# Kernel optimization log

Hardware: AMD Instinct MI355X
Metric: run time of the kernel (lower is better)

## Reference

```python
import jax, jax.numpy as jnp
import numpy as np

N, D, C, P = 4096, 512, 100, 64
EPS_COS = 1e-8   # torch cosine_similarity norm clamp
EPS_INV = 1e-5   # module's 1/(d + 1e-5)


def setup_inputs() -> dict:
    key = jax.random.key(0)
    k1, k2, k3, k4 = jax.random.split(key, 4)
    feats = jax.random.normal(k1, (N, D), dtype=jnp.float32)
    protos = jax.random.normal(k2, (C, P, D), dtype=jnp.float32)
    cls_ids = jax.random.randint(k3, (N,), 0, C)
    proto_labels = jax.random.randint(k4, (C, P), 0, 1000)
    return {"feats": feats, "protos": protos, "cls_ids": cls_ids,
            "proto_labels": proto_labels}


def reference(feats, protos, cls_ids, proto_labels):
    # Gather each box's class-conditional prototype set: [N, P, D]
    p = protos[cls_ids]
    pl = proto_labels[cls_ids]                       # [N, P]

    # cosine distance: 1 - f.p / (max(|f|,eps) * max(|p|,eps))
    dot = jnp.einsum('nd,npd->np', feats, p)         # [N, P]
    fnorm = jnp.maximum(jnp.linalg.norm(feats, axis=-1, keepdims=True), EPS_COS)
    pnorm = jnp.maximum(jnp.linalg.norm(p, axis=-1), EPS_COS)
    d_cos = 1.0 - dot / (fnorm * pnorm)

    diff = feats[:, None, :] - p                     # [N, P, D]
    d_l1 = jnp.mean(jnp.abs(diff), axis=-1)          # F.l1_loss (mean)
    d_l2 = jnp.mean(diff * diff, axis=-1)            # F.mse_loss (mean)

    dists = jnp.stack([d_cos, d_l1, d_l2], axis=1)   # [N, 3, P]
    probs = jax.nn.softmax(1.0 / (dists + EPS_INV), axis=-1).mean(axis=1)  # [N, P]

    idx = jnp.argmax(probs, axis=-1)                 # [N]
    labels = jnp.take_along_axis(pl, idx[:, None], axis=1)[:, 0]
    return labels, probs
```

## Files before the change

kernel.cpp:

```cpp
#include <hip/hip_runtime.h>

#define D 512
#define P 64
#define CHUNK 16
#define MAXDESC 512
#define EPS_COS 1e-8f
#define EPS_INV 1e-5f


__device__ __forceinline__ float wave_sum(float v) {
#pragma unroll
    for (int m = 32; m >= 1; m >>= 1) v += __shfl_xor(v, m, 64);
    return v;
}

__global__ __launch_bounds__(256) void proto_norm_kernel(
    const float* __restrict__ protos, float* __restrict__ pp, int rows)
{
    const int lane = threadIdx.x & 63;
    const int r = blockIdx.x * 4 + (threadIdx.x >> 6);
    if (r >= rows) return;
    const float* row = protos + (size_t)r * D;
    const float4 a = *(const float4*)(row + lane * 4);
    const float4 b = *(const float4*)(row + 256 + lane * 4);
    float s = a.x*a.x + a.y*a.y + a.z*a.z + a.w*a.w
            + b.x*b.x + b.y*b.y + b.z*b.z + b.w*b.w;
    s = wave_sum(s);
    if (lane == 0) pp[r] = s;
}

__global__ __launch_bounds__(256) void hist_kernel(
    const int* __restrict__ cls, int* counts, int N)
{
    const int n = blockIdx.x * 256 + threadIdx.x;
    if (n < N) atomicAdd(&counts[cls[n]], 1);
}

__global__ __launch_bounds__(64) void scan_desc_kernel(
    const int* __restrict__ counts, int* base, int* desc, int* ndesc, int C)
{
    const int lane = threadIdx.x;
    const int c0 = lane, c1 = lane + 64;
    const int v0 = (c0 < C) ? counts[c0] : 0;
    const int v1 = (c1 < C) ? counts[c1] : 0;
    int s0 = v0, s1 = v1;
#pragma unroll
    for (int d = 1; d < 64; d <<= 1) {
        int t = __shfl_up(s0, d, 64); if (lane >= d) s0 += t;
        t     = __shfl_up(s1, d, 64); if (lane >= d) s1 += t;
    }
    s1 += __shfl(s0, 63, 64);
    const int b0 = s0 - v0, b1 = s1 - v1;
    if (c0 < C) base[c0] = b0;
    if (c1 < C) base[c1] = b1;

    const int g0 = (v0 + CHUNK - 1) / CHUNK, g1 = (v1 + CHUNK - 1) / CHUNK;
    int t0 = g0, t1 = g1;
#pragma unroll
    for (int d = 1; d < 64; d <<= 1) {
        int t = __shfl_up(t0, d, 64); if (lane >= d) t0 += t;
        t     = __shfl_up(t1, d, 64); if (lane >= d) t1 += t;
    }
    t1 += __shfl(t0, 63, 64);
    const int go0 = t0 - g0, go1 = t1 - g1;
    if (lane == 63) ndesc[0] = t1;
    for (int k = 0; k < g0; ++k) {
        const int di = go0 + k;
        desc[3*di] = c0; desc[3*di+1] = b0 + CHUNK*k; desc[3*di+2] = min(CHUNK, v0 - CHUNK*k);
    }
    for (int k = 0; k < g1; ++k) {
        const int di = go1 + k;
        desc[3*di] = c1; desc[3*di+1] = b1 + CHUNK*k; desc[3*di+2] = min(CHUNK, v1 - CHUNK*k);
    }
}

__global__ __launch_bounds__(256) void scatter_kernel(
    const int* __restrict__ cls, const int* __restrict__ base,
    int* fill, int* sorted, int N)
{
    const int n = blockIdx.x * 256 + threadIdx.x;
    if (n < N) {
        const int c = cls[n];
        const int pos = base[c] + atomicAdd(&fill[c], 1);
        sorted[pos] = n;
    }
}

__global__ __launch_bounds__(256, 2) void proto_main_kernel(
    const float* __restrict__ feats,
    const float* __restrict__ protos,
    const int*   __restrict__ proto_labels,
    const float* __restrict__ ppbuf,
    const int*   __restrict__ sorted,
    const int*   __restrict__ desc,
    const int*   __restrict__ ndesc,
    float* __restrict__ out, int N)
{
    __shared__ float tile[32 * D];
    const int nd = ndesc[0];
    if ((int)blockIdx.x >= nd) return;
    const int cls   = desc[3*blockIdx.x];
    const int start = desc[3*blockIdx.x+1];
    const int cnt   = desc[3*blockIdx.x+2];
    const int lane = threadIdx.x & 63;
    const int wave = threadIdx.x >> 6;

    int  nidx[4];
    bool valid[4];
#pragma unroll
    for (int k = 0; k < 4; ++k) {
        const int pos = wave + 4*k;
        valid[k] = pos < cnt;
        nidx[k]  = sorted[start + (valid[k] ? pos : (cnt - 1))];
    }

    float4 f0[4], f1[4];
    float  ff[4];
#pragma unroll
    for (int b = 0; b < 4; ++b) {
        const float* f = feats + (size_t)nidx[b] * D;
        f0[b] = *(const float4*)(f + lane * 4);
        f1[b] = *(const float4*)(f + 256 + lane * 4);
        float s = f0[b].x*f0[b].x + f0[b].y*f0[b].y + f0[b].z*f0[b].z + f0[b].w*f0[b].w
                + f1[b].x*f1[b].x + f1[b].y*f1[b].y + f1[b].z*f1[b].z + f1[b].w*f1[b].w;
        ff[b] = wave_sum(s);
    }

    const float* pr = protos + (size_t)cls * (P * D);
    const int jsel = (lane >> 3) & 7;
    const int gown = lane & 7;
    const bool hi32 = (lane & 32) != 0;
    const bool hi16 = (lane & 16) != 0;
    const bool hi8  = (lane & 8)  != 0;

    float r_dot[4] = {0.f,0.f,0.f,0.f}, r_l1[4] = {0.f,0.f,0.f,0.f};

    for (int pass = 0; pass < 2; ++pass) {
#pragma unroll
        for (int k = 0; k < 16; ++k) {
            const int idx = threadIdx.x + 256 * k;
            *(float4*)(tile + idx * 4) =
                *(const float4*)(pr + pass * (32 * D) + idx * 4);
        }
        __syncthreads();

        for (int gl = 0; gl < 4; ++gl) {
            const int g = pass * 4 + gl;
            float pd[4][8], pl[4][8];
#pragma unroll
            for (int j = 0; j < 8; ++j) {
                const float* row = tile + (gl * 8 + j) * D;
                const float4 q0 = *(const float4*)(row + lane * 4);
                const float4 q1 = *(const float4*)(row + 256 + lane * 4);
#pragma unroll
                for (int b = 0; b < 4; ++b) {
                    float dot, l1, t;
                    dot  = f0[b].x*q0.x; t = f0[b].x - q0.x; l1  = fabsf(t);
                    dot += f0[b].y*q0.y; t = f0[b].y - q0.y; l1 += fabsf(t);
                    dot += f0[b].z*q0.z; t = f0[b].z - q0.z; l1 += fabsf(t);
                    dot += f0[b].w*q0.w; t = f0[b].w - q0.w; l1 += fabsf(t);
                    dot += f1[b].x*q1.x; t = f1[b].x - q1.x; l1 += fabsf(t);
                    dot += f1[b].y*q1.y; t = f1[b].y - q1.y; l1 += fabsf(t);
                    dot += f1[b].z*q1.z; t = f1[b].z - q1.z; l1 += fabsf(t);
                    dot += f1[b].w*q1.w; t = f1[b].w - q1.w; l1 += fabsf(t);
                    pd[b][j] = dot; pl[b][j] = l1;
                }
            }
#pragma unroll
            for (int b = 0; b < 4; ++b) {
#pragma unroll
                for (int k = 0; k < 4; ++k) {
                    const float sd = hi32 ? pd[b][k] : pd[b][k+4];
                    const float sl = hi32 ? pl[b][k] : pl[b][k+4];
                    const float rd = __shfl_xor(sd, 32, 64);
                    const float rl = __shfl_xor(sl, 32, 64);
                    pd[b][k] = (hi32 ? pd[b][k+4] : pd[b][k]) + rd;
                    pl[b][k] = (hi32 ? pl[b][k+4] : pl[b][k]) + rl;
                }
#pragma unroll
                for (int k = 0; k < 2; ++k) {
                    const float sd = hi16 ? pd[b][k] : pd[b][k+2];
                    const float sl = hi16 ? pl[b][k] : pl[b][k+2];
                    const float rd = __shfl_xor(sd, 16, 64);
                    const float rl = __shfl_xor(sl, 16, 64);
                    pd[b][k] = (hi16 ? pd[b][k+2] : pd[b][k]) + rd;
                    pl[b][k] = (hi16 ? pl[b][k+2] : pl[b][k]) + rl;
                }
                {
                    const float sd = hi8 ? pd[b][0] : pd[b][1];
                    const float sl = hi8 ? pl[b][0] : pl[b][1];
                    const float rd = __shfl_xor(sd, 8, 64);
                    const float rl = __shfl_xor(sl, 8, 64);
                    pd[b][0] = (hi8 ? pd[b][1] : pd[b][0]) + rd;
                    pl[b][0] = (hi8 ? pl[b][1] : pl[b][0]) + rl;
                }
#pragma unroll
                for (int m = 4; m >= 1; m >>= 1) {
                    pd[b][0] += __shfl_xor(pd[b][0], m, 64);
                    pl[b][0] += __shfl_xor(pl[b][0], m, 64);
                }
                if (gown == g) { r_dot[b] = pd[b][0]; r_l1[b] = pl[b][0]; }
            }
        }
        __syncthreads();
    }

    const int myp = 8 * gown + jsel;
    const float s_pp = ppbuf[cls * P + myp];

#pragma unroll
    for (int b = 0; b < 4; ++b) {
        const float fnorm = fmaxf(sqrtf(ff[b]), EPS_COS);
        const float pnorm = fmaxf(sqrtf(s_pp),  EPS_COS);
        const float d_cos = 1.0f - r_dot[b] / (fnorm * pnorm);
        const float d_l1  = r_l1[b] * (1.0f / (float)D);
        const float d_l2  = (ff[b] - 2.0f * r_dot[b] + s_pp) * (1.0f / (float)D);

        float s[3];
        s[0] = 1.0f / (d_cos + EPS_INV);
        s[1] = 1.0f / (d_l1  + EPS_INV);
        s[2] = 1.0f / (d_l2  + EPS_INV);

        float prob = 0.f;
#pragma unroll
        for (int i = 0; i < 3; ++i) {
            float m = s[i];
#pragma unroll
            for (int w = 32; w >= 1; w >>= 1) m = fmaxf(m, __shfl_xor(m, w, 64));
            const float e = expf(s[i] - m);
            prob += e / wave_sum(e);
        }
        prob *= (1.0f / 3.0f);

        float best = prob;
        int   bidx = myp;
#pragma unroll
        for (int w = 32; w >= 1; w >>= 1) {
            const float ov = __shfl_xor(best, w, 64);
            const int   oi = __shfl_xor(bidx, w, 64);
            if (ov > best || (ov == best && oi < bidx)) { best = ov; bidx = oi; }
        }

        if (valid[b]) {
            out[(size_t)N + (size_t)nidx[b] * P + myp] = prob;
            if (lane == 0) out[nidx[b]] = (float)proto_labels[cls * P + bidx];
        }
    }
}

extern "C" void kernel_launch(void* const* d_in, const int* in_sizes, int n_in,
                              void* d_out, int out_size, void* d_ws, size_t ws_size,
                              hipStream_t stream) {
    const float* feats        = (const float*)d_in[0];
    const float* protos       = (const float*)d_in[1];
    const int*   cls_ids      = (const int*)d_in[2];
    const int*   proto_labels = (const int*)d_in[3];
    float* out = (float*)d_out;

    const int N    = in_sizes[2];
    const int rows = in_sizes[1] / D;
    const int C    = rows / P;

    char* w = (char*)d_ws;
    float* pp     = (float*)w;
    int*   counts = (int*)(w + 25600);
    int*   fill   = (int*)(w + 26112);
    int*   base   = (int*)(w + 26624);
    int*   ndesc  = (int*)(w + 27136);
    int*   desc   = (int*)(w + 27200);
    int*   sorted = (int*)(w + 33344);

    hipMemsetAsync(counts, 0, 1024, stream);
    proto_norm_kernel<<<(rows + 3) / 4, 256, 0, stream>>>(protos, pp, rows);
    hist_kernel<<<(N + 255) / 256, 256, 0, stream>>>(cls_ids, counts, N);
    scan_desc_kernel<<<1, 64, 0, stream>>>(counts, base, desc, ndesc, C);
    scatter_kernel<<<(N + 255) / 256, 256, 0, stream>>>(cls_ids, base, fill, sorted, N);
    proto_main_kernel<<<MAXDESC, 256, 0, stream>>>(
        feats, protos, proto_labels, pp, sorted, desc, ndesc, out, N);
}
```

Baseline: 128.1 us.

## Fuse sort setup into one block kernel and split prototypes across 8 waves

```diff
diff --git a/kernel.cpp b/kernel.cpp
--- a/kernel.cpp
+++ b/kernel.cpp
@@ -3,7 +3,7 @@
 #define D 512
 #define P 64
 #define CHUNK 16
-#define MAXDESC 512
+#define MAXDESC 384
 #define EPS_COS 1e-8f
 #define EPS_INV 1e-5f
 
@@ -29,64 +29,54 @@
     if (lane == 0) pp[r] = s;
 }
 
-__global__ __launch_bounds__(256) void hist_kernel(
-    const int* __restrict__ cls, int* counts, int N)
+__global__ __launch_bounds__(1024) void setup_kernel(
+    const int* __restrict__ cls, int* __restrict__ sorted,
+    int* __restrict__ desc, int* __restrict__ ndesc, int N, int C)
 {
-    const int n = blockIdx.x * 256 + threadIdx.x;
-    if (n < N) atomicAdd(&counts[cls[n]], 1);
-}
-
-__global__ __launch_bounds__(64) void scan_desc_kernel(
-    const int* __restrict__ counts, int* base, int* desc, int* ndesc, int C)
-{
-    const int lane = threadIdx.x;
-    const int c0 = lane, c1 = lane + 64;
-    const int v0 = (c0 < C) ? counts[c0] : 0;
-    const int v1 = (c1 < C) ? counts[c1] : 0;
-    int s0 = v0, s1 = v1;
-#pragma unroll
-    for (int d = 1; d < 64; d <<= 1) {
-        int t = __shfl_up(s0, d, 64); if (lane >= d) s0 += t;
-        t     = __shfl_up(s1, d, 64); if (lane >= d) s1 += t;
-    }
-    s1 += __shfl(s0, 63, 64);
-    const int b0 = s0 - v0, b1 = s1 - v1;
-    if (c0 < C) base[c0] = b0;
-    if (c1 < C) base[c1] = b1;
-
-    const int g0 = (v0 + CHUNK - 1) / CHUNK, g1 = (v1 + CHUNK - 1) / CHUNK;
-    int t0 = g0, t1 = g1;
-#pragma unroll
-    for (int d = 1; d < 64; d <<= 1) {
-        int t = __shfl_up(t0, d, 64); if (lane >= d) t0 += t;
-        t     = __shfl_up(t1, d, 64); if (lane >= d) t1 += t;
-    }
-    t1 += __shfl(t0, 63, 64);
-    const int go0 = t0 - g0, go1 = t1 - g1;
-    if (lane == 63) ndesc[0] = t1;
-    for (int k = 0; k < g0; ++k) {
-        const int di = go0 + k;
-        desc[3*di] = c0; desc[3*di+1] = b0 + CHUNK*k; desc[3*di+2] = min(CHUNK, v0 - CHUNK*k);
-    }
-    for (int k = 0; k < g1; ++k) {
-        const int di = go1 + k;
-        desc[3*di] = c1; desc[3*di+1] = b1 + CHUNK*k; desc[3*di+2] = min(CHUNK, v1 - CHUNK*k);
-    }
-}
-
-__global__ __launch_bounds__(256) void scatter_kernel(
-    const int* __restrict__ cls, const int* __restrict__ base,
-    int* fill, int* sorted, int N)
-{
-    const int n = blockIdx.x * 256 + threadIdx.x;
-    if (n < N) {
-        const int c = cls[n];
-        const int pos = base[c] + atomicAdd(&fill[c], 1);
-        sorted[pos] = n;
-    }
-}
-
-__global__ __launch_bounds__(256, 2) void proto_main_kernel(
+    __shared__ int cnt[128], fl[128], exc[128], gexc[128];
+    const int t = threadIdx.x;
+    if (t < 128) { cnt[t] = 0; fl[t] = 0; }
+    __syncthreads();
+#pragma unroll
+    for (int k = 0; k < 4; ++k) {
+        const int n = t + 1024 * k;
+        if (n < N) atomicAdd(&cnt[cls[n]], 1);
+    }
+    __syncthreads();
+    int v = 0, gv = 0;
+    if (t < 128) { v = cnt[t]; gv = (v + CHUNK - 1) / CHUNK; exc[t] = v; gexc[t] = gv; }
+    __syncthreads();
+    for (int d = 1; d < 128; d <<= 1) {
+        int a = 0, b = 0;
+        if (t < 128 && t >= d) { a = exc[t - d]; b = gexc[t - d]; }
+        __syncthreads();
+        if (t < 128 && t >= d) { exc[t] += a; gexc[t] += b; }
+        __syncthreads();
+    }
+    int base = 0, gbase = 0;
+    if (t < 128) { base = exc[t] - v; gbase = gexc[t] - gv; }
+    if (t == 127) ndesc[0] = gexc[127];
+    if (t < 128) exc[t] = base;
+    __syncthreads();
+    if (t < C) {
+        for (int k = 0; k < gv; ++k) {
+            desc[3*(gbase+k)+0] = t;
+            desc[3*(gbase+k)+1] = base + CHUNK*k;
+            desc[3*(gbase+k)+2] = min(CHUNK, v - CHUNK*k);
+        }
+    }
+#pragma unroll
+    for (int k = 0; k < 4; ++k) {
+        const int n = t + 1024 * k;
+        if (n < N) {
+            const int c = cls[n];
+            const int pos = exc[c] + atomicAdd(&fl[c], 1);
+            sorted[pos] = n;
+        }
+    }
+}
+
+__global__ __launch_bounds__(512, 2) void proto_main_kernel(
     const float* __restrict__ feats,
     const float* __restrict__ protos,
     const int*   __restrict__ proto_labels,
@@ -96,22 +86,25 @@
     const int*   __restrict__ ndesc,
     float* __restrict__ out, int N)
 {
-    __shared__ float tile[32 * D];
-    const int nd = ndesc[0];
-    if ((int)blockIdx.x >= nd) return;
+    __shared__ float tile[16 * D];
+    __shared__ float dist[CHUNK * P * 2];
+    __shared__ float ffbuf[CHUNK];
+
+    if ((int)blockIdx.x >= ndesc[0]) return;
     const int cls   = desc[3*blockIdx.x];
     const int start = desc[3*blockIdx.x+1];
     const int cnt   = desc[3*blockIdx.x+2];
-    const int lane = threadIdx.x & 63;
-    const int wave = threadIdx.x >> 6;
-
-    int  nidx[4];
-    bool valid[4];
+    const int tid  = threadIdx.x;
+    const int lane = tid & 63;
+    const int wave = tid >> 6;
+    const int bg = wave & 3;
+    const int h  = wave >> 2;
+
+    int nidx[4];
 #pragma unroll
     for (int k = 0; k < 4; ++k) {
-        const int pos = wave + 4*k;
-        valid[k] = pos < cnt;
-        nidx[k]  = sorted[start + (valid[k] ? pos : (cnt - 1))];
+        const int pos = bg + 4*k;
+        nidx[k] = sorted[start + (pos < cnt ? pos : cnt - 1)];
     }
 
     float4 f0[4], f1[4];
@@ -125,115 +118,128 @@
                 + f1[b].x*f1[b].x + f1[b].y*f1[b].y + f1[b].z*f1[b].z + f1[b].w*f1[b].w;
         ff[b] = wave_sum(s);
     }
+    if (h == 0 && lane == 0) {
+#pragma unroll
+        for (int k = 0; k < 4; ++k) ffbuf[bg + 4*k] = ff[k];
+    }
 
     const float* pr = protos + (size_t)cls * (P * D);
-    const int jsel = (lane >> 3) & 7;
-    const int gown = lane & 7;
     const bool hi32 = (lane & 32) != 0;
     const bool hi16 = (lane & 16) != 0;
     const bool hi8  = (lane & 8)  != 0;
 
     float r_dot[4] = {0.f,0.f,0.f,0.f}, r_l1[4] = {0.f,0.f,0.f,0.f};
 
-    for (int pass = 0; pass < 2; ++pass) {
-#pragma unroll
-        for (int k = 0; k < 16; ++k) {
-            const int idx = threadIdx.x + 256 * k;
+    for (int pass = 0; pass < 4; ++pass) {
+        if (pass) __syncthreads();
+#pragma unroll
+        for (int i = 0; i < 4; ++i) {
+            const int idx = tid + 512 * i;
             *(float4*)(tile + idx * 4) =
-                *(const float4*)(pr + pass * (32 * D) + idx * 4);
+                *(const float4*)(pr + pass * (16 * D) + idx * 4);
         }
         __syncthreads();
 
-        for (int gl = 0; gl < 4; ++gl) {
-            const int g = pass * 4 + gl;
-            float pd[4][8], pl[4][8];
-#pragma unroll
-            for (int j = 0; j < 8; ++j) {
-                const float* row = tile + (gl * 8 + j) * D;
-                const float4 q0 = *(const float4*)(row + lane * 4);
-                const float4 q1 = *(const float4*)(row + 256 + lane * 4);
-#pragma unroll
-                for (int b = 0; b < 4; ++b) {
-                    float dot, l1, t;
-                    dot  = f0[b].x*q0.x; t = f0[b].x - q0.x; l1  = fabsf(t);
-                    dot += f0[b].y*q0.y; t = f0[b].y - q0.y; l1 += fabsf(t);
-                    dot += f0[b].z*q0.z; t = f0[b].z - q0.z; l1 += fabsf(t);
-                    dot += f0[b].w*q0.w; t = f0[b].w - q0.w; l1 += fabsf(t);
-                    dot += f1[b].x*q1.x; t = f1[b].x - q1.x; l1 += fabsf(t);
-                    dot += f1[b].y*q1.y; t = f1[b].y - q1.y; l1 += fabsf(t);
-                    dot += f1[b].z*q1.z; t = f1[b].z - q1.z; l1 += fabsf(t);
-                    dot += f1[b].w*q1.w; t = f1[b].w - q1.w; l1 += fabsf(t);
-                    pd[b][j] = dot; pl[b][j] = l1;
-                }
-            }
+        float pd[4][8], pl[4][8];
+#pragma unroll
+        for (int j = 0; j < 8; ++j) {
+            const float* row = tile + (8 * h + j) * D;
+            const float4 q0 = *(const float4*)(row + lane * 4);
+            const float4 q1 = *(const float4*)(row + 256 + lane * 4);
 #pragma unroll
             for (int b = 0; b < 4; ++b) {
-#pragma unroll
-                for (int k = 0; k < 4; ++k) {
-                    const float sd = hi32 ? pd[b][k] : pd[b][k+4];
-                    const float sl = hi32 ? pl[b][k] : pl[b][k+4];
-                    const float rd = __shfl_xor(sd, 32, 64);
-                    const float rl = __shfl_xor(sl, 32, 64);
-                    pd[b][k] = (hi32 ? pd[b][k+4] : pd[b][k]) + rd;
-                    pl[b][k] = (hi32 ? pl[b][k+4] : pl[b][k]) + rl;
-                }
-#pragma unroll
-                for (int k = 0; k < 2; ++k) {
-                    const float sd = hi16 ? pd[b][k] : pd[b][k+2];
-                    const float sl = hi16 ? pl[b][k] : pl[b][k+2];
-                    const float rd = __shfl_xor(sd, 16, 64);
-                    const float rl = __shfl_xor(sl, 16, 64);
-                    pd[b][k] = (hi16 ? pd[b][k+2] : pd[b][k]) + rd;
-                    pl[b][k] = (hi16 ? pl[b][k+2] : pl[b][k]) + rl;
-                }
-                {
-                    const float sd = hi8 ? pd[b][0] : pd[b][1];
-                    const float sl = hi8 ? pl[b][0] : pl[b][1];
-                    const float rd = __shfl_xor(sd, 8, 64);
-                    const float rl = __shfl_xor(sl, 8, 64);
-                    pd[b][0] = (hi8 ? pd[b][1] : pd[b][0]) + rd;
-                    pl[b][0] = (hi8 ? pl[b][1] : pl[b][0]) + rl;
-                }
-#pragma unroll
-                for (int m = 4; m >= 1; m >>= 1) {
-                    pd[b][0] += __shfl_xor(pd[b][0], m, 64);
-                    pl[b][0] += __shfl_xor(pl[b][0], m, 64);
-                }
-                if (gown == g) { r_dot[b] = pd[b][0]; r_l1[b] = pl[b][0]; }
-            }
-        }
-        __syncthreads();
-    }
-
-    const int myp = 8 * gown + jsel;
-    const float s_pp = ppbuf[cls * P + myp];
-
-#pragma unroll
-    for (int b = 0; b < 4; ++b) {
-        const float fnorm = fmaxf(sqrtf(ff[b]), EPS_COS);
-        const float pnorm = fmaxf(sqrtf(s_pp),  EPS_COS);
-        const float d_cos = 1.0f - r_dot[b] / (fnorm * pnorm);
-        const float d_l1  = r_l1[b] * (1.0f / (float)D);
-        const float d_l2  = (ff[b] - 2.0f * r_dot[b] + s_pp) * (1.0f / (float)D);
-
-        float s[3];
-        s[0] = 1.0f / (d_cos + EPS_INV);
-        s[1] = 1.0f / (d_l1  + EPS_INV);
-        s[2] = 1.0f / (d_l2  + EPS_INV);
+                float dot, l1, t;
+                dot  = f0[b].x*q0.x; t = f0[b].x - q0.x; l1  = fabsf(t);
+                dot += f0[b].y*q0.y; t = f0[b].y - q0.y; l1 += fabsf(t);
+                dot += f0[b].z*q0.z; t = f0[b].z - q0.z; l1 += fabsf(t);
+                dot += f0[b].w*q0.w; t = f0[b].w - q0.w; l1 += fabsf(t);
+                dot += f1[b].x*q1.x; t = f1[b].x - q1.x; l1 += fabsf(t);
+                dot += f1[b].y*q1.y; t = f1[b].y - q1.y; l1 += fabsf(t);
+                dot += f1[b].z*q1.z; t = f1[b].z - q1.z; l1 += fabsf(t);
+                dot += f1[b].w*q1.w; t = f1[b].w - q1.w; l1 += fabsf(t);
+                pd[b][j] = dot; pl[b][j] = l1;
+            }
+        }
+#pragma unroll
+        for (int b = 0; b < 4; ++b) {
+#pragma unroll
+            for (int k = 0; k < 4; ++k) {
+                const float sd = hi32 ? pd[b][k] : pd[b][k+4];
+                const float sl = hi32 ? pl[b][k] : pl[b][k+4];
+                const float rd = __shfl_xor(sd, 32, 64);
+                const float rl = __shfl_xor(sl, 32, 64);
+                pd[b][k] = (hi32 ? pd[b][k+4] : pd[b][k]) + rd;
+                pl[b][k] = (hi32 ? pl[b][k+4] : pl[b][k]) + rl;
+            }
+#pragma unroll
+            for (int k = 0; k < 2; ++k) {
+                const float sd = hi16 ? pd[b][k] : pd[b][k+2];
+                const float sl = hi16 ? pl[b][k] : pl[b][k+2];
+                const float rd = __shfl_xor(sd, 16, 64);
+                const float rl = __shfl_xor(sl, 16, 64);
+                pd[b][k] = (hi16 ? pd[b][k+2] : pd[b][k]) + rd;
+                pl[b][k] = (hi16 ? pl[b][k+2] : pl[b][k]) + rl;
+            }
+            {
+                const float sd = hi8 ? pd[b][0] : pd[b][1];
+                const float sl = hi8 ? pl[b][0] : pl[b][1];
+                const float rd = __shfl_xor(sd, 8, 64);
+                const float rl = __shfl_xor(sl, 8, 64);
+                pd[b][0] = (hi8 ? pd[b][1] : pd[b][0]) + rd;
+                pl[b][0] = (hi8 ? pl[b][1] : pl[b][0]) + rl;
+            }
+#pragma unroll
+            for (int m = 4; m >= 1; m >>= 1) {
+                pd[b][0] += __shfl_xor(pd[b][0], m, 64);
+                pl[b][0] += __shfl_xor(pl[b][0], m, 64);
+            }
+            if ((lane & 3) == pass) { r_dot[b] = pd[b][0]; r_l1[b] = pl[b][0]; }
+        }
+    }
+
+    {
+        const int pg   = 16 * (lane & 3) + 8 * h + ((lane >> 3) & 7);
+        const int qsel = (lane >> 2) & 1;
+#pragma unroll
+        for (int k = 0; k < 4; ++k) {
+            dist[((bg + 4*k) * P + pg) * 2 + qsel] = qsel ? r_l1[k] : r_dot[k];
+        }
+    }
+    __syncthreads();
+
+    const float ppv   = ppbuf[cls * P + lane];
+    const float pnorm = fmaxf(sqrtf(ppv), EPS_COS);
+
+#pragma unroll
+    for (int kk = 0; kk < 2; ++kk) {
+        const int s = 2 * wave + kk;
+        if (s >= cnt) continue;
+        const int n = sorted[start + s];
+        const float2 dl = *(const float2*)&dist[(s * P + lane) * 2];
+        const float ffv   = ffbuf[s];
+        const float fnorm = fmaxf(sqrtf(ffv), EPS_COS);
+        const float d_cos = 1.0f - dl.x / (fnorm * pnorm);
+        const float d_l1  = dl.y * (1.0f / (float)D);
+        const float d_l2  = (ffv - 2.0f * dl.x + ppv) * (1.0f / (float)D);
+
+        float sc[3];
+        sc[0] = 1.0f / (d_cos + EPS_INV);
+        sc[1] = 1.0f / (d_l1  + EPS_INV);
+        sc[2] = 1.0f / (d_l2  + EPS_INV);
 
         float prob = 0.f;
 #pragma unroll
         for (int i = 0; i < 3; ++i) {
-            float m = s[i];
+            float m = sc[i];
 #pragma unroll
             for (int w = 32; w >= 1; w >>= 1) m = fmaxf(m, __shfl_xor(m, w, 64));
-            const float e = expf(s[i] - m);
+            const float e = expf(sc[i] - m);
             prob += e / wave_sum(e);
         }
         prob *= (1.0f / 3.0f);
 
         float best = prob;
-        int   bidx = myp;
+        int   bidx = lane;
 #pragma unroll
         for (int w = 32; w >= 1; w >>= 1) {
             const float ov = __shfl_xor(best, w, 64);
@@ -241,10 +247,8 @@
             if (ov > best || (ov == best && oi < bidx)) { best = ov; bidx = oi; }
         }
 
-        if (valid[b]) {
-            out[(size_t)N + (size_t)nidx[b] * P + myp] = prob;
-            if (lane == 0) out[nidx[b]] = (float)proto_labels[cls * P + bidx];
-        }
+        out[(size_t)N + (size_t)n * P + lane] = prob;
+        if (lane == 0) out[n] = (float)proto_labels[cls * P + bidx];
     }
 }
 
@@ -263,18 +267,12 @@
 
     char* w = (char*)d_ws;
     float* pp     = (float*)w;
-    int*   counts = (int*)(w + 25600);
-    int*   fill   = (int*)(w + 26112);
-    int*   base   = (int*)(w + 26624);
-    int*   ndesc  = (int*)(w + 27136);
-    int*   desc   = (int*)(w + 27200);
-    int*   sorted = (int*)(w + 33344);
-
-    hipMemsetAsync(counts, 0, 1024, stream);
+    int*   sorted = (int*)(w + 25600);
+    int*   desc   = (int*)(w + 41984);
+    int*   ndesc  = (int*)(w + 46592);
+
     proto_norm_kernel<<<(rows + 3) / 4, 256, 0, stream>>>(protos, pp, rows);
-    hist_kernel<<<(N + 255) / 256, 256, 0, stream>>>(cls_ids, counts, N);
-    scan_desc_kernel<<<1, 64, 0, stream>>>(counts, base, desc, ndesc, C);
-    scatter_kernel<<<(N + 255) / 256, 256, 0, stream>>>(cls_ids, base, fill, sorted, N);
-    proto_main_kernel<<<MAXDESC, 256, 0, stream>>>(
+    setup_kernel<<<1, 1024, 0, stream>>>(cls_ids, sorted, desc, ndesc, N, C);
+    proto_main_kernel<<<MAXDESC, 512, 0, stream>>>(
         feats, protos, proto_labels, pp, sorted, desc, ndesc, out, N);
 }
```

Measured after the change: 123.3 us. 1.04x faster.
